# Optimization experiments

Hardware: AMD Instinct MI355X
Metric: run time of the kernel (lower is better)

Reference implementation:

```python
import jax, jax.numpy as jnp
import numpy as np
import math

SQ, SK, B, NP, HN = 2048, 2048, 2, 16, 128
LAYER_NUM = 1  # coeff
NORM_FACTOR = math.sqrt(2048 / 16) * LAYER_NUM  # sqrt(HIDDEN/HEADS) * coeff
SCALE = float(LAYER_NUM)  # MLSASoftmax scale


def setup_inputs() -> dict:
    key = jax.random.key(0)
    kq, kk, kv = jax.random.split(key, 3)
    query_layer = jax.random.normal(kq, (SQ, B, NP, HN), dtype=jnp.float32)
    key_layer = jax.random.normal(kk, (SK, B, NP, HN), dtype=jnp.float32)
    value_layer = jax.random.normal(kv, (SK, B, NP, HN), dtype=jnp.float32)
    # Causal mask: True = masked, shape [b, 1, sq, sk] (broadcasts over heads)
    causal = jnp.triu(jnp.ones((SQ, SK), dtype=bool), k=1)
    attention_mask = jnp.broadcast_to(causal[None, None], (B, 1, SQ, SK))
    return {
        "query_layer": query_layer,
        "key_layer": key_layer,
        "value_layer": value_layer,
        "attention_mask": attention_mask,
    }


def reference(query_layer, key_layer, value_layer, attention_mask):
    # scores[b,n,s,t] = (Q . K) / norm_factor, then * coeff in softmax
    scores = jnp.einsum("sbnh,tbnh->bnst", query_layer, key_layer) / NORM_FACTOR
    scores = scores * SCALE
    scores = jnp.where(attention_mask, jnp.float32(-10000.0), scores)
    # Module computes exp/sum WITHOUT max-subtraction; replicate exactly.
    exp_mo = jnp.exp(scores)
    denomi = jnp.sum(exp_mo, axis=-1, keepdims=True)  # [b, np, sq, 1]
    probs = exp_mo / denomi
    # dropout is identity in eval / for deterministic baseline
    ctx = jnp.einsum("bnst,tbnh->sbnh", probs, value_layer)  # [sq, b, np, hn]
    sq, b, n, h = ctx.shape
    context_layer = ctx.reshape(sq, b, n * h)
    return (context_layer, denomi)
```

## Files before the change

kernel.cpp:

```cpp
#include <hip/hip_runtime.h>
#include <hip/hip_bf16.h>
#include <stdint.h>

typedef __attribute__((ext_vector_type(8))) short short8;
typedef __attribute__((ext_vector_type(8))) unsigned short ushort8;
typedef __attribute__((ext_vector_type(4))) float f32x4;
typedef __attribute__((ext_vector_type(4))) int int4v;

#define NHEAD 32
#define SEQ   2048
#define HN    128

static constexpr float INV_NORM = 0.08838834764831845f;

__device__ __forceinline__ unsigned short f2bf(float f) {
  union { float f; unsigned u; } v; v.f = f;
  unsigned r = v.u + 0x7fffu + ((v.u >> 16) & 1u);
  return (unsigned short)(r >> 16);
}

__device__ __forceinline__ f32x4 mfma16(short8 a, short8 b, f32x4 c) {
  return __builtin_amdgcn_mfma_f32_16x16x32_bf16(a, b, c, 0, 0, 0);
}

__device__ __forceinline__ void gl_lds16(const void* g, void* l) {
  __builtin_amdgcn_global_load_lds(
      (const __attribute__((address_space(1))) unsigned int*)g,
      (__attribute__((address_space(3))) unsigned int*)l, 16, 0, 0);
}

__global__ __launch_bounds__(256) void prep_kv(const float* __restrict__ K,
                                               const float* __restrict__ V,
                                               unsigned short* __restrict__ kswz,
                                               unsigned short* __restrict__ vT) {
  __shared__ unsigned short lds[128 * 136];
  int bid = blockIdx.x;
  int tid = threadIdx.x;
  if (bid < 4096) {
    int idx = bid * 256 + tid;
    int cl = idx & 15;
    int t  = (idx >> 4) & 2047;
    int bn = idx >> 15;
    const float4* src = (const float4*)(K + ((size_t)t * 32 + bn) * 128 + cl * 8);
    float4 a = src[0], b = src[1];
    ushort8 o;
    o[0]=f2bf(a.x); o[1]=f2bf(a.y); o[2]=f2bf(a.z); o[3]=f2bf(a.w);
    o[4]=f2bf(b.x); o[5]=f2bf(b.y); o[6]=f2bf(b.z); o[7]=f2bf(b.w);
    *(ushort8*)(kswz + ((size_t)bn * 2048 + t) * 128 + ((cl ^ (t & 7)) * 8)) = o;
  } else {
    int vb = bid - 4096;
    int bn = vb >> 4;
    int t0 = (vb & 15) << 7;
    int r = tid >> 1, h0 = (tid & 1) * 64;
    const float* src = V + ((size_t)(t0 + r) * 32 + bn) * 128 + h0;
#pragma unroll
    for (int j = 0; j < 8; ++j) {
      float4 a = *(const float4*)(src + j * 8);
      float4 b = *(const float4*)(src + j * 8 + 4);
      ushort8 o;
      o[0]=f2bf(a.x); o[1]=f2bf(a.y); o[2]=f2bf(a.z); o[3]=f2bf(a.w);
      o[4]=f2bf(b.x); o[5]=f2bf(b.y); o[6]=f2bf(b.z); o[7]=f2bf(b.w);
      *(ushort8*)&lds[r * 136 + h0 + j * 8] = o;
    }
    __syncthreads();
    int h = tid >> 1, ts = (tid & 1) * 64;
    unsigned short tmp[64];
#pragma unroll
    for (int j = 0; j < 64; ++j) {
      int p = j & 31;
      int tloc = ((p >> 3) & 3) * 4 + ((p >> 2) & 1) * 16 + (p & 3);
      tmp[j] = lds[(ts + (j & 32) + tloc) * 136 + h];
    }
    ushort8* dst = (ushort8*)(vT + ((size_t)bn * 128 + h) * 2048 + t0 + ts);
#pragma unroll
    for (int j = 0; j < 8; ++j) dst[j] = *(ushort8*)&tmp[j * 8];
  }
}

template<bool BOTH>
__device__ __forceinline__ void half_tile(
    const char* kb, const char* vbh, int halfbase, int t0h, int qh, int ql,
    int l15, int hi, const short8 (&qf)[2][4],
    f32x4 (&acc)[2][8], float (&dacc)[2]) {
  f32x4 zz = {0.f, 0.f, 0.f, 0.f};
  int xr = (l15 & 7) << 4;
  short8 kf[2][4];
#pragma unroll
  for (int nt = 0; nt < 2; ++nt) {
    const char* krow = kb + (halfbase + nt * 16 + l15) * 256;
#pragma unroll
    for (int kk = 0; kk < 4; ++kk)
      kf[nt][kk] = *(const short8*)(krow + (((kk * 4 + hi) * 16) ^ xr));
  }
  f32x4 sH[2] = {zz, zz}, sL[2] = {zz, zz};
  __builtin_amdgcn_s_setprio(1);
#pragma unroll
  for (int nt = 0; nt < 2; ++nt)
#pragma unroll
    for (int kk = 0; kk < 4; ++kk) {
      sH[nt] = mfma16(kf[nt][kk], qf[0][kk], sH[nt]);
      if (BOTH) sL[nt] = mfma16(kf[nt][kk], qf[1][kk], sL[nt]);
    }
  __builtin_amdgcn_s_setprio(0);
  short8 vf[8];
#pragma unroll
  for (int ht = 0; ht < 8; ++ht)
    vf[ht] = *(const short8*)(vbh + (ht * 16 + l15) * 64 +
                              ((((l15 >> 1) + hi) & 3) * 16));
  auto pack = [&](float (&e)[8], float& da) -> short8 {
    da += ((e[0] + e[1]) + (e[2] + e[3])) + ((e[4] + e[5]) + (e[6] + e[7]));
    unsigned w0, w1, w2, w3;
    asm("v_cvt_pk_bf16_f32 %0, %1, %2" : "=v"(w0) : "v"(e[0]), "v"(e[1]));
    asm("v_cvt_pk_bf16_f32 %0, %1, %2" : "=v"(w1) : "v"(e[2]), "v"(e[3]));
    asm("v_cvt_pk_bf16_f32 %0, %1, %2" : "=v"(w2) : "v"(e[4]), "v"(e[5]));
    asm("v_cvt_pk_bf16_f32 %0, %1, %2" : "=v"(w3) : "v"(e[6]), "v"(e[7]));
    union { int4v u; short8 s; } pk;
    pk.u = (int4v){(int)w0, (int)w1, (int)w2, (int)w3};
    return pk.s;
  };
  auto softp_m = [&](f32x4* sv, int qbase, float& da) -> short8 {
    float e[8];
#pragma unroll
    for (int nt = 0; nt < 2; ++nt)
#pragma unroll
      for (int i = 0; i < 4; ++i) {
        float x = __expf(sv[nt][i] * INV_NORM);
        int kv = t0h + nt * 16 + hi * 4 + i;
        e[nt * 4 + i] = (kv <= qbase + l15) ? x : 0.0f;
      }
    return pack(e, da);
  };
  auto softp_u = [&](f32x4* sv, float& da) -> short8 {
    float e[8];
#pragma unroll
    for (int nt = 0; nt < 2; ++nt)
#pragma unroll
      for (int i = 0; i < 4; ++i)
        e[nt * 4 + i] = __expf(sv[nt][i] * INV_NORM);
    return pack(e, da);
  };
  bool maskH = (t0h + 31 > qh);
  short8 pH = maskH ? softp_m(sH, qh, dacc[0]) : softp_u(sH, dacc[0]);
  short8 pL = {};
  if (BOTH) {
    bool maskL = (t0h + 31 > ql);
    pL = maskL ? softp_m(sL, ql, dacc[1]) : softp_u(sL, dacc[1]);
  }
  __builtin_amdgcn_s_setprio(1);
#pragma unroll
  for (int ht = 0; ht < 8; ++ht) {
    acc[0][ht] = mfma16(pH, vf[ht], acc[0][ht]);
    if (BOTH) acc[1][ht] = mfma16(pL, vf[ht], acc[1][ht]);
  }
  __builtin_amdgcn_s_setprio(0);
}

__global__ __launch_bounds__(256, 2) void attn_main(const float* __restrict__ Q,
                                                    const unsigned short* __restrict__ kswz,
                                                    const unsigned short* __restrict__ vT,
                                                    float* __restrict__ out) {
  __shared__ char smem[65536];
  int tid = threadIdx.x;
  int lane = tid & 63;
  int w = tid >> 6;
  int l15 = lane & 15;
  int hi = lane >> 4;

  int bid = blockIdx.x;
  int bn = bid & 31;
  int x = bid >> 5;
  int p = (x < 8) ? x : 23 - x;
  int qtH = 31 - p, qtL = p;
  int qh = qtH * 64 + w * 16;
  int ql = qtL * 64 + w * 16;
  int ntile = qtH + 1;

  short8 qf[2][4];
#pragma unroll
  for (int qs = 0; qs < 2; ++qs) {
    int qbase = qs ? ql : qh;
    const float* qrow = Q + ((size_t)(qbase + l15) * 32 + bn) * 128;
#pragma unroll
    for (int kk = 0; kk < 4; ++kk) {
      float4 a = *(const float4*)(qrow + kk * 32 + hi * 8);
      float4 b = *(const float4*)(qrow + kk * 32 + hi * 8 + 4);
      short8 o;
      o[0]=(short)f2bf(a.x); o[1]=(short)f2bf(a.y);
      o[2]=(short)f2bf(a.z); o[3]=(short)f2bf(a.w);
      o[4]=(short)f2bf(b.x); o[5]=(short)f2bf(b.y);
      o[6]=(short)f2bf(b.z); o[7]=(short)f2bf(b.w);
      qf[qs][kk] = o;
    }
  }

  f32x4 zz = {0.f, 0.f, 0.f, 0.f};
  f32x4 acc[2][8];
#pragma unroll
  for (int qs = 0; qs < 2; ++qs)
#pragma unroll
    for (int ht = 0; ht < 8; ++ht) acc[qs][ht] = zz;
  float dacc[2] = {0.f, 0.f};

  const char* kg = (const char*)(kswz + (size_t)bn * 2048 * 128);
  const char* vg = (const char*)(vT + (size_t)bn * 128 * 2048);

  auto stage = [&](int buf, int t0) {
    const char* ksrc = kg + (size_t)t0 * 256;
    char* kl = smem + buf * 16384;
    int c = w * 64 + lane;
#pragma unroll
    for (int rr = 0; rr < 4; ++rr)
      gl_lds16(ksrc + (size_t)(c + rr * 256) * 16, kl + (c + rr * 256) * 16);
    char* vl = smem + 32768 + buf * 16384;
#pragma unroll
    for (int s = 0; s < 2; ++s)
#pragma unroll
      for (int rr = 0; rr < 2; ++rr) {
        int c2 = c + rr * 256;
        int h = c2 >> 2, sp = c2 & 3;
        int sl = (sp - (h >> 1)) & 3;
        gl_lds16(vg + (size_t)h * 4096 + (t0 + s * 32) * 2 + sl * 16,
                 vl + s * 8192 + c2 * 16);
      }
  };

  asm volatile("s_waitcnt vmcnt(0)" ::: "memory");
  stage(0, 0);

  int cur = 0;
  for (int it = 0; it < ntile; ++it) {
    int t0 = it * 64;
    asm volatile("s_waitcnt vmcnt(0)" ::: "memory");
    __builtin_amdgcn_s_barrier();
    if (it + 1 < ntile) stage(cur ^ 1, t0 + 64);

    const char* kb = smem + cur * 16384;
    const char* vb = smem + 32768 + cur * 16384;
#pragma unroll
    for (int half = 0; half < 2; ++half) {
      int t0h = t0 + half * 32;
      bool actL = (t0h <= ql + 15);
      bool actH = (t0h <= qh + 15);
      if (actL)
        half_tile<true>(kb, vb + half * 8192, half * 32, t0h, qh, ql,
                        l15, hi, qf, acc, dacc);
      else if (actH)
        half_tile<false>(kb, vb + half * 8192, half * 32, t0h, qh, ql,
                         l15, hi, qf, acc, dacc);
    }
    cur ^= 1;
  }

#pragma unroll
  for (int qs = 0; qs < 2; ++qs) {
    float d = dacc[qs];
    d += __shfl_xor(d, 16);
    d += __shfl_xor(d, 32);
    dacc[qs] = d;
  }
  float* dn = out + 8388608;
  if (hi == 0) {
    dn[(size_t)bn * 2048 + qh + l15] = dacc[0];
    dn[(size_t)bn * 2048 + ql + l15] = dacc[1];
  }
  float invH[4], invL[4];
#pragma unroll
  for (int i = 0; i < 4; ++i) {
    invH[i] = __builtin_amdgcn_rcpf(__shfl(dacc[0], hi * 4 + i));
    invL[i] = __builtin_amdgcn_rcpf(__shfl(dacc[1], hi * 4 + i));
  }

#pragma unroll
  for (int qs = 0; qs < 2; ++qs) {
    int qbase = qs ? ql : qh;
#pragma unroll
    for (int i = 0; i < 4; ++i) {
      float inv = qs ? invL[i] : invH[i];
      float* orow = out + (size_t)(qbase + hi * 4 + i) * 4096 + bn * 128 + l15;
#pragma unroll
      for (int ht = 0; ht < 8; ++ht)
        orow[ht * 16] = acc[qs][ht][i] * inv;
    }
  }
}

extern "C" void kernel_launch(void* const* d_in, const int* in_sizes, int n_in,
                              void* d_out, int out_size, void* d_ws, size_t ws_size,
                              hipStream_t stream) {
  const float* Q = (const float*)d_in[0];
  const float* K = (const float*)d_in[1];
  const float* V = (const float*)d_in[2];
  float* out = (float*)d_out;

  unsigned short* kswz = (unsigned short*)d_ws;
  unsigned short* vT   = kswz + (size_t)NHEAD * SEQ * HN;

  prep_kv<<<4608, 256, 0, stream>>>(K, V, kswz, vT);
  attn_main<<<512, 256, 0, stream>>>(Q, kswz, vT, out);
}
```

Before: 82.39 us.

## Split KV sequence across two wave groups per block and reduce partials in LDS

Doubles the block to 512 threads, with two groups of four waves each handling alternating 32-key half tiles of the same query rows, each with its own double-buffered LDS region. At the end the partial denominators and output accumulators are combined through shared memory before the normalized write. The aim is to raise the number of resident waves and hide latency within a block, in exchange for extra reduction traffic, more barriers, and heavier register pressure under the new launch bounds.

```diff
diff --git a/kernel.cpp b/kernel.cpp
--- a/kernel.cpp
+++ b/kernel.cpp
@@ -79,7 +79,7 @@
 
 template<bool BOTH>
 __device__ __forceinline__ void half_tile(
-    const char* kb, const char* vbh, int halfbase, int t0h, int qh, int ql,
+    const char* kb, const char* vbh, int t0h, int qh, int ql,
     int l15, int hi, const short8 (&qf)[2][4],
     f32x4 (&acc)[2][8], float (&dacc)[2]) {
   f32x4 zz = {0.f, 0.f, 0.f, 0.f};
@@ -87,7 +87,7 @@
   short8 kf[2][4];
 #pragma unroll
   for (int nt = 0; nt < 2; ++nt) {
-    const char* krow = kb + (halfbase + nt * 16 + l15) * 256;
+    const char* krow = kb + (nt * 16 + l15) * 256;
 #pragma unroll
     for (int kk = 0; kk < 4; ++kk)
       kf[nt][kk] = *(const short8*)(krow + (((kk * 4 + hi) * 16) ^ xr));
@@ -155,14 +155,16 @@
   __builtin_amdgcn_s_setprio(0);
 }
 
-__global__ __launch_bounds__(256, 2) void attn_main(const float* __restrict__ Q,
+__global__ __launch_bounds__(512, 4) void attn_main(const float* __restrict__ Q,
                                                     const unsigned short* __restrict__ kswz,
                                                     const unsigned short* __restrict__ vT,
                                                     float* __restrict__ out) {
   __shared__ char smem[65536];
   int tid = threadIdx.x;
   int lane = tid & 63;
-  int w = tid >> 6;
+  int w8 = tid >> 6;
+  int w = w8 & 3;
+  int sid = w8 >> 2;
   int l15 = lane & 15;
   int hi = lane >> 4;
 
@@ -173,7 +175,7 @@
   int qtH = 31 - p, qtL = p;
   int qh = qtH * 64 + w * 16;
   int ql = qtL * 64 + w * 16;
-  int ntile = qtH + 1;
+  int nIt = qtH + 1;
 
   short8 qf[2][4];
 #pragma unroll
@@ -204,52 +206,79 @@
   const char* kg = (const char*)(kswz + (size_t)bn * 2048 * 128);
   const char* vg = (const char*)(vT + (size_t)bn * 128 * 2048);
 
-  auto stage = [&](int buf, int t0) {
-    const char* ksrc = kg + (size_t)t0 * 256;
-    char* kl = smem + buf * 16384;
+  char* kbase = smem + sid * 16384;
+  char* vbase = smem + 32768 + sid * 16384;
+
+  auto stage = [&](int buf, int t) {
+    const char* ksrc = kg + (size_t)t * 8192;
+    char* kl = kbase + buf * 8192;
     int c = w * 64 + lane;
 #pragma unroll
-    for (int rr = 0; rr < 4; ++rr)
+    for (int rr = 0; rr < 2; ++rr)
       gl_lds16(ksrc + (size_t)(c + rr * 256) * 16, kl + (c + rr * 256) * 16);
-    char* vl = smem + 32768 + buf * 16384;
-#pragma unroll
-    for (int s = 0; s < 2; ++s)
-#pragma unroll
-      for (int rr = 0; rr < 2; ++rr) {
-        int c2 = c + rr * 256;
-        int h = c2 >> 2, sp = c2 & 3;
-        int sl = (sp - (h >> 1)) & 3;
-        gl_lds16(vg + (size_t)h * 4096 + (t0 + s * 32) * 2 + sl * 16,
-                 vl + s * 8192 + c2 * 16);
-      }
+    char* vl = vbase + buf * 8192;
+#pragma unroll
+    for (int rr = 0; rr < 2; ++rr) {
+      int c2 = c + rr * 256;
+      int h = c2 >> 2, sp = c2 & 3;
+      int sl = (sp - (h >> 1)) & 3;
+      gl_lds16(vg + (size_t)h * 4096 + (size_t)t * 64 + sl * 16,
+               vl + c2 * 16);
+    }
   };
 
   asm volatile("s_waitcnt vmcnt(0)" ::: "memory");
-  stage(0, 0);
+  stage(0, sid);
 
   int cur = 0;
-  for (int it = 0; it < ntile; ++it) {
-    int t0 = it * 64;
+  for (int it = 0; it < nIt; ++it) {
+    int t = it * 2 + sid;
     asm volatile("s_waitcnt vmcnt(0)" ::: "memory");
     __builtin_amdgcn_s_barrier();
-    if (it + 1 < ntile) stage(cur ^ 1, t0 + 64);
-
-    const char* kb = smem + cur * 16384;
-    const char* vb = smem + 32768 + cur * 16384;
-#pragma unroll
-    for (int half = 0; half < 2; ++half) {
-      int t0h = t0 + half * 32;
-      bool actL = (t0h <= ql + 15);
-      bool actH = (t0h <= qh + 15);
-      if (actL)
-        half_tile<true>(kb, vb + half * 8192, half * 32, t0h, qh, ql,
-                        l15, hi, qf, acc, dacc);
-      else if (actH)
-        half_tile<false>(kb, vb + half * 8192, half * 32, t0h, qh, ql,
-                         l15, hi, qf, acc, dacc);
-    }
+    if (it + 1 < nIt) stage(cur ^ 1, t + 2);
+
+    int t0h = t * 32;
+    const char* kb = kbase + cur * 8192;
+    const char* vbh = vbase + cur * 8192;
+    bool actL = (t0h <= ql + 15);
+    bool actH = (t0h <= qh + 15);
+    if (actL)
+      half_tile<true>(kb, vbh, t0h, qh, ql, l15, hi, qf, acc, dacc);
+    else if (actH)
+      half_tile<false>(kb, vbh, t0h, qh, ql, l15, hi, qf, acc, dacc);
     cur ^= 1;
   }
+
+  __syncthreads();
+  float* dsm = (float*)smem;
+  if (sid == 1) {
+    dsm[0 * 256 + w * 64 + lane] = dacc[0];
+    dsm[1 * 256 + w * 64 + lane] = dacc[1];
+  }
+  __syncthreads();
+  if (sid == 0) {
+    dacc[0] += dsm[0 * 256 + w * 64 + lane];
+    dacc[1] += dsm[1 * 256 + w * 64 + lane];
+  }
+  __syncthreads();
+  f32x4* accsm = (f32x4*)smem;
+  if (sid == 1) {
+#pragma unroll
+    for (int qs = 0; qs < 2; ++qs)
+#pragma unroll
+      for (int ht = 0; ht < 8; ++ht)
+        accsm[(qs * 8 + ht) * 256 + w * 64 + lane] = acc[qs][ht];
+  }
+  __syncthreads();
+  if (sid == 1) return;
+#pragma unroll
+  for (int qs = 0; qs < 2; ++qs)
+#pragma unroll
+    for (int ht = 0; ht < 8; ++ht) {
+      f32x4 o = accsm[(qs * 8 + ht) * 256 + w * 64 + lane];
+      acc[qs][ht][0] += o[0]; acc[qs][ht][1] += o[1];
+      acc[qs][ht][2] += o[2]; acc[qs][ht][3] += o[3];
+    }
 
 #pragma unroll
   for (int qs = 0; qs < 2; ++qs) {
@@ -296,5 +325,5 @@
   unsigned short* vT   = kswz + (size_t)NHEAD * SEQ * HN;
 
   prep_kv<<<4608, 256, 0, stream>>>(K, V, kswz, vT);
-  attn_main<<<512, 256, 0, stream>>>(Q, kswz, vT, out);
-}
+  attn_main<<<512, 512, 0, stream>>>(Q, kswz, vT, out);
+}
```

New measurement: 255.0 us. 3.1x slower.

## Interleave QK and PV MFMAs across two half-tiles and fold scale into Q

Applied to the files above, without the earlier changes.

Adds a tile64 path that processes both 32-key halves of a 64-key tile together, computing the second half's QK scores while the first half's softmax and PV MFMAs run. This lets exp/pack work overlap with matrix ops. The first K fragment is now read from LDS before the next async stage is issued. The 1/sqrt(d) scale is folded into Q before its bf16 conversion, which removes a multiply per score but changes rounding slightly. Register pressure rises from holding two score sets and two V fragment sets, which may hurt occupancy at launch bounds of 2.

```diff
diff --git a/kernel.cpp b/kernel.cpp
--- a/kernel.cpp
+++ b/kernel.cpp
@@ -77,21 +77,70 @@
   }
 }
 
+__device__ __forceinline__ void read_kf(const char* kb, int base, int l15, int hi,
+                                        short8 (&kf)[2][4]) {
+  int xr = (l15 & 7) << 4;
+#pragma unroll
+  for (int nt = 0; nt < 2; ++nt) {
+    const char* krow = kb + (base + nt * 16 + l15) * 256;
+#pragma unroll
+    for (int kk = 0; kk < 4; ++kk)
+      kf[nt][kk] = *(const short8*)(krow + (((kk * 4 + hi) * 16) ^ xr));
+  }
+}
+
+__device__ __forceinline__ void read_vf(const char* vbh, int l15, int hi,
+                                        short8 (&vf)[8]) {
+#pragma unroll
+  for (int ht = 0; ht < 8; ++ht)
+    vf[ht] = *(const short8*)(vbh + (ht * 16 + l15) * 64 +
+                              ((((l15 >> 1) + hi) & 3) * 16));
+}
+
+__device__ __forceinline__ short8 packp(const float (&e)[8], float& da) {
+  da += ((e[0] + e[1]) + (e[2] + e[3])) + ((e[4] + e[5]) + (e[6] + e[7]));
+  unsigned w0, w1, w2, w3;
+  asm("v_cvt_pk_bf16_f32 %0, %1, %2" : "=v"(w0) : "v"(e[0]), "v"(e[1]));
+  asm("v_cvt_pk_bf16_f32 %0, %1, %2" : "=v"(w1) : "v"(e[2]), "v"(e[3]));
+  asm("v_cvt_pk_bf16_f32 %0, %1, %2" : "=v"(w2) : "v"(e[4]), "v"(e[5]));
+  asm("v_cvt_pk_bf16_f32 %0, %1, %2" : "=v"(w3) : "v"(e[6]), "v"(e[7]));
+  union { int4v u; short8 s; } pk;
+  pk.u = (int4v){(int)w0, (int)w1, (int)w2, (int)w3};
+  return pk.s;
+}
+
+__device__ __forceinline__ short8 softp_m(const f32x4 (&sv)[2], int t0h, int qbase,
+                                          int l15, int hi, float& da) {
+  float e[8];
+#pragma unroll
+  for (int nt = 0; nt < 2; ++nt)
+#pragma unroll
+    for (int i = 0; i < 4; ++i) {
+      float x = __expf(sv[nt][i]);
+      int kv = t0h + nt * 16 + hi * 4 + i;
+      e[nt * 4 + i] = (kv <= qbase + l15) ? x : 0.0f;
+    }
+  return packp(e, da);
+}
+
+__device__ __forceinline__ short8 softp_u(const f32x4 (&sv)[2], float& da) {
+  float e[8];
+#pragma unroll
+  for (int nt = 0; nt < 2; ++nt)
+#pragma unroll
+    for (int i = 0; i < 4; ++i)
+      e[nt * 4 + i] = __expf(sv[nt][i]);
+  return packp(e, da);
+}
+
 template<bool BOTH>
 __device__ __forceinline__ void half_tile(
     const char* kb, const char* vbh, int halfbase, int t0h, int qh, int ql,
     int l15, int hi, const short8 (&qf)[2][4],
     f32x4 (&acc)[2][8], float (&dacc)[2]) {
   f32x4 zz = {0.f, 0.f, 0.f, 0.f};
-  int xr = (l15 & 7) << 4;
   short8 kf[2][4];
-#pragma unroll
-  for (int nt = 0; nt < 2; ++nt) {
-    const char* krow = kb + (halfbase + nt * 16 + l15) * 256;
-#pragma unroll
-    for (int kk = 0; kk < 4; ++kk)
-      kf[nt][kk] = *(const short8*)(krow + (((kk * 4 + hi) * 16) ^ xr));
-  }
+  read_kf(kb, halfbase, l15, hi, kf);
   f32x4 sH[2] = {zz, zz}, sL[2] = {zz, zz};
   __builtin_amdgcn_s_setprio(1);
 #pragma unroll
@@ -103,54 +152,82 @@
     }
   __builtin_amdgcn_s_setprio(0);
   short8 vf[8];
-#pragma unroll
-  for (int ht = 0; ht < 8; ++ht)
-    vf[ht] = *(const short8*)(vbh + (ht * 16 + l15) * 64 +
-                              ((((l15 >> 1) + hi) & 3) * 16));
-  auto pack = [&](float (&e)[8], float& da) -> short8 {
-    da += ((e[0] + e[1]) + (e[2] + e[3])) + ((e[4] + e[5]) + (e[6] + e[7]));
-    unsigned w0, w1, w2, w3;
-    asm("v_cvt_pk_bf16_f32 %0, %1, %2" : "=v"(w0) : "v"(e[0]), "v"(e[1]));
-    asm("v_cvt_pk_bf16_f32 %0, %1, %2" : "=v"(w1) : "v"(e[2]), "v"(e[3]));
-    asm("v_cvt_pk_bf16_f32 %0, %1, %2" : "=v"(w2) : "v"(e[4]), "v"(e[5]));
-    asm("v_cvt_pk_bf16_f32 %0, %1, %2" : "=v"(w3) : "v"(e[6]), "v"(e[7]));
-    union { int4v u; short8 s; } pk;
-    pk.u = (int4v){(int)w0, (int)w1, (int)w2, (int)w3};
-    return pk.s;
-  };
-  auto softp_m = [&](f32x4* sv, int qbase, float& da) -> short8 {
-    float e[8];
-#pragma unroll
-    for (int nt = 0; nt < 2; ++nt)
-#pragma unroll
-      for (int i = 0; i < 4; ++i) {
-        float x = __expf(sv[nt][i] * INV_NORM);
-        int kv = t0h + nt * 16 + hi * 4 + i;
-        e[nt * 4 + i] = (kv <= qbase + l15) ? x : 0.0f;
-      }
-    return pack(e, da);
-  };
-  auto softp_u = [&](f32x4* sv, float& da) -> short8 {
-    float e[8];
-#pragma unroll
-    for (int nt = 0; nt < 2; ++nt)
-#pragma unroll
-      for (int i = 0; i < 4; ++i)
-        e[nt * 4 + i] = __expf(sv[nt][i] * INV_NORM);
-    return pack(e, da);
-  };
+  read_vf(vbh, l15, hi, vf);
   bool maskH = (t0h + 31 > qh);
-  short8 pH = maskH ? softp_m(sH, qh, dacc[0]) : softp_u(sH, dacc[0]);
+  short8 pH = maskH ? softp_m(sH, t0h, qh, l15, hi, dacc[0]) : softp_u(sH, dacc[0]);
   short8 pL = {};
   if (BOTH) {
     bool maskL = (t0h + 31 > ql);
-    pL = maskL ? softp_m(sL, ql, dacc[1]) : softp_u(sL, dacc[1]);
+    pL = maskL ? softp_m(sL, t0h, ql, l15, hi, dacc[1]) : softp_u(sL, dacc[1]);
   }
   __builtin_amdgcn_s_setprio(1);
 #pragma unroll
   for (int ht = 0; ht < 8; ++ht) {
     acc[0][ht] = mfma16(pH, vf[ht], acc[0][ht]);
     if (BOTH) acc[1][ht] = mfma16(pL, vf[ht], acc[1][ht]);
+  }
+  __builtin_amdgcn_s_setprio(0);
+}
+
+template<bool BOTH>
+__device__ __forceinline__ void tile64(
+    const char* kb, const char* vb, int t0, int qh, int ql,
+    int l15, int hi, const short8 (&qf)[2][4], const short8 (&kf0)[2][4],
+    f32x4 (&acc)[2][8], float (&dacc)[2]) {
+  f32x4 zz = {0.f, 0.f, 0.f, 0.f};
+  f32x4 sH0[2] = {zz, zz}, sL0[2] = {zz, zz};
+  __builtin_amdgcn_s_setprio(1);
+#pragma unroll
+  for (int nt = 0; nt < 2; ++nt)
+#pragma unroll
+    for (int kk = 0; kk < 4; ++kk) {
+      sH0[nt] = mfma16(kf0[nt][kk], qf[0][kk], sH0[nt]);
+      if (BOTH) sL0[nt] = mfma16(kf0[nt][kk], qf[1][kk], sL0[nt]);
+    }
+  __builtin_amdgcn_s_setprio(0);
+  short8 kf1[2][4];
+  read_kf(kb, 32, l15, hi, kf1);
+  short8 vf0[8];
+  read_vf(vb, l15, hi, vf0);
+  f32x4 sH1[2] = {zz, zz}, sL1[2] = {zz, zz};
+  __builtin_amdgcn_s_setprio(1);
+#pragma unroll
+  for (int nt = 0; nt < 2; ++nt)
+#pragma unroll
+    for (int kk = 0; kk < 4; ++kk) {
+      sH1[nt] = mfma16(kf1[nt][kk], qf[0][kk], sH1[nt]);
+      if (BOTH) sL1[nt] = mfma16(kf1[nt][kk], qf[1][kk], sL1[nt]);
+    }
+  bool mH0 = (t0 + 31 > qh);
+  short8 pH0 = mH0 ? softp_m(sH0, t0, qh, l15, hi, dacc[0]) : softp_u(sH0, dacc[0]);
+  short8 pL0 = {};
+  if (BOTH) {
+    bool mL0 = (t0 + 31 > ql);
+    pL0 = mL0 ? softp_m(sL0, t0, ql, l15, hi, dacc[1]) : softp_u(sL0, dacc[1]);
+  }
+  __builtin_amdgcn_s_setprio(0);
+  short8 vf1[8];
+  read_vf(vb + 8192, l15, hi, vf1);
+  int t1 = t0 + 32;
+  __builtin_amdgcn_s_setprio(1);
+#pragma unroll
+  for (int ht = 0; ht < 8; ++ht) {
+    acc[0][ht] = mfma16(pH0, vf0[ht], acc[0][ht]);
+    if (BOTH) acc[1][ht] = mfma16(pL0, vf0[ht], acc[1][ht]);
+  }
+  bool mH1 = (t1 + 31 > qh);
+  short8 pH1 = mH1 ? softp_m(sH1, t1, qh, l15, hi, dacc[0]) : softp_u(sH1, dacc[0]);
+  short8 pL1 = {};
+  if (BOTH) {
+    bool mL1 = (t1 + 31 > ql);
+    pL1 = mL1 ? softp_m(sL1, t1, ql, l15, hi, dacc[1]) : softp_u(sL1, dacc[1]);
+  }
+  __builtin_amdgcn_s_setprio(0);
+  __builtin_amdgcn_s_setprio(1);
+#pragma unroll
+  for (int ht = 0; ht < 8; ++ht) {
+    acc[0][ht] = mfma16(pH1, vf1[ht], acc[0][ht]);
+    if (BOTH) acc[1][ht] = mfma16(pL1, vf1[ht], acc[1][ht]);
   }
   __builtin_amdgcn_s_setprio(0);
 }
@@ -185,10 +262,10 @@
       float4 a = *(const float4*)(qrow + kk * 32 + hi * 8);
       float4 b = *(const float4*)(qrow + kk * 32 + hi * 8 + 4);
       short8 o;
-      o[0]=(short)f2bf(a.x); o[1]=(short)f2bf(a.y);
-      o[2]=(short)f2bf(a.z); o[3]=(short)f2bf(a.w);
-      o[4]=(short)f2bf(b.x); o[5]=(short)f2bf(b.y);
-      o[6]=(short)f2bf(b.z); o[7]=(short)f2bf(b.w);
+      o[0]=(short)f2bf(a.x*INV_NORM); o[1]=(short)f2bf(a.y*INV_NORM);
+      o[2]=(short)f2bf(a.z*INV_NORM); o[3]=(short)f2bf(a.w*INV_NORM);
+      o[4]=(short)f2bf(b.x*INV_NORM); o[5]=(short)f2bf(b.y*INV_NORM);
+      o[6]=(short)f2bf(b.z*INV_NORM); o[7]=(short)f2bf(b.w*INV_NORM);
       qf[qs][kk] = o;
     }
   }
@@ -232,21 +309,33 @@
     int t0 = it * 64;
     asm volatile("s_waitcnt vmcnt(0)" ::: "memory");
     __builtin_amdgcn_s_barrier();
-    if (it + 1 < ntile) stage(cur ^ 1, t0 + 64);
 
     const char* kb = smem + cur * 16384;
     const char* vb = smem + 32768 + cur * 16384;
-#pragma unroll
-    for (int half = 0; half < 2; ++half) {
-      int t0h = t0 + half * 32;
-      bool actL = (t0h <= ql + 15);
-      bool actH = (t0h <= qh + 15);
-      if (actL)
-        half_tile<true>(kb, vb + half * 8192, half * 32, t0h, qh, ql,
-                        l15, hi, qf, acc, dacc);
-      else if (actH)
-        half_tile<false>(kb, vb + half * 8192, half * 32, t0h, qh, ql,
-                         l15, hi, qf, acc, dacc);
+    bool L0 = (t0 <= ql + 15);
+    bool L1 = (t0 + 32 <= ql + 15);
+    bool H1 = (t0 + 32 <= qh + 15);
+
+    if (L1 || (!L0 && H1)) {
+      short8 kf0[2][4];
+      read_kf(kb, 0, l15, hi, kf0);
+      if (it + 1 < ntile) stage(cur ^ 1, t0 + 64);
+      if (L1) tile64<true>(kb, vb, t0, qh, ql, l15, hi, qf, kf0, acc, dacc);
+      else    tile64<false>(kb, vb, t0, qh, ql, l15, hi, qf, kf0, acc, dacc);
+    } else {
+      if (it + 1 < ntile) stage(cur ^ 1, t0 + 64);
+#pragma unroll
+      for (int half = 0; half < 2; ++half) {
+        int t0h = t0 + half * 32;
+        bool actL = (t0h <= ql + 15);
+        bool actH = (t0h <= qh + 15);
+        if (actL)
+          half_tile<true>(kb, vb + half * 8192, half * 32, t0h, qh, ql,
+                          l15, hi, qf, acc, dacc);
+        else if (actH)
+          half_tile<false>(kb, vb + half * 8192, half * 32, t0h, qh, ql,
+                           l15, hi, qf, acc, dacc);
+      }
     }
     cur ^= 1;
   }
```

Result: no change. 82.70 us (+0.4%).

## Split paired query tiles into single-tile blocks with smaller LDS and higher occupancy

Applied to the files above, without the earlier changes.

Each block previously handled a causal-balanced pair of query tiles (high and low) using 64-row K/V stages. Now each block handles one 64-row query tile with 32-key stages. Grid size doubles, LDS is halved, and launch bounds allow 4 blocks per CU. The block order is arranged so the longest tiles launch first, replacing the old pairing for load balance. The softmax scale is folded into Q at load, and the K fragment read is moved ahead of issuing the next stage. The cost is that each K/V tile is now loaded twice as often per query row and there are more barriers per unit of work.

```diff
diff --git a/kernel.cpp b/kernel.cpp
--- a/kernel.cpp
+++ b/kernel.cpp
@@ -77,89 +77,67 @@
   }
 }
 
-template<bool BOTH>
-__device__ __forceinline__ void half_tile(
-    const char* kb, const char* vbh, int halfbase, int t0h, int qh, int ql,
-    int l15, int hi, const short8 (&qf)[2][4],
-    f32x4 (&acc)[2][8], float (&dacc)[2]) {
-  f32x4 zz = {0.f, 0.f, 0.f, 0.f};
+__device__ __forceinline__ void read_kf(const char* kb, int l15, int hi,
+                                        short8 (&kf)[2][4]) {
   int xr = (l15 & 7) << 4;
-  short8 kf[2][4];
 #pragma unroll
   for (int nt = 0; nt < 2; ++nt) {
-    const char* krow = kb + (halfbase + nt * 16 + l15) * 256;
+    const char* krow = kb + (nt * 16 + l15) * 256;
 #pragma unroll
     for (int kk = 0; kk < 4; ++kk)
       kf[nt][kk] = *(const short8*)(krow + (((kk * 4 + hi) * 16) ^ xr));
   }
-  f32x4 sH[2] = {zz, zz}, sL[2] = {zz, zz};
-  __builtin_amdgcn_s_setprio(1);
-#pragma unroll
-  for (int nt = 0; nt < 2; ++nt)
-#pragma unroll
-    for (int kk = 0; kk < 4; ++kk) {
-      sH[nt] = mfma16(kf[nt][kk], qf[0][kk], sH[nt]);
-      if (BOTH) sL[nt] = mfma16(kf[nt][kk], qf[1][kk], sL[nt]);
-    }
-  __builtin_amdgcn_s_setprio(0);
-  short8 vf[8];
+}
+
+__device__ __forceinline__ void read_vf(const char* vbh, int l15, int hi,
+                                        short8 (&vf)[8]) {
 #pragma unroll
   for (int ht = 0; ht < 8; ++ht)
     vf[ht] = *(const short8*)(vbh + (ht * 16 + l15) * 64 +
                               ((((l15 >> 1) + hi) & 3) * 16));
-  auto pack = [&](float (&e)[8], float& da) -> short8 {
-    da += ((e[0] + e[1]) + (e[2] + e[3])) + ((e[4] + e[5]) + (e[6] + e[7]));
-    unsigned w0, w1, w2, w3;
-    asm("v_cvt_pk_bf16_f32 %0, %1, %2" : "=v"(w0) : "v"(e[0]), "v"(e[1]));
-    asm("v_cvt_pk_bf16_f32 %0, %1, %2" : "=v"(w1) : "v"(e[2]), "v"(e[3]));
-    asm("v_cvt_pk_bf16_f32 %0, %1, %2" : "=v"(w2) : "v"(e[4]), "v"(e[5]));
-    asm("v_cvt_pk_bf16_f32 %0, %1, %2" : "=v"(w3) : "v"(e[6]), "v"(e[7]));
-    union { int4v u; short8 s; } pk;
-    pk.u = (int4v){(int)w0, (int)w1, (int)w2, (int)w3};
-    return pk.s;
-  };
-  auto softp_m = [&](f32x4* sv, int qbase, float& da) -> short8 {
-    float e[8];
-#pragma unroll
-    for (int nt = 0; nt < 2; ++nt)
-#pragma unroll
-      for (int i = 0; i < 4; ++i) {
-        float x = __expf(sv[nt][i] * INV_NORM);
-        int kv = t0h + nt * 16 + hi * 4 + i;
-        e[nt * 4 + i] = (kv <= qbase + l15) ? x : 0.0f;
-      }
-    return pack(e, da);
-  };
-  auto softp_u = [&](f32x4* sv, float& da) -> short8 {
-    float e[8];
-#pragma unroll
-    for (int nt = 0; nt < 2; ++nt)
-#pragma unroll
-      for (int i = 0; i < 4; ++i)
-        e[nt * 4 + i] = __expf(sv[nt][i] * INV_NORM);
-    return pack(e, da);
-  };
-  bool maskH = (t0h + 31 > qh);
-  short8 pH = maskH ? softp_m(sH, qh, dacc[0]) : softp_u(sH, dacc[0]);
-  short8 pL = {};
-  if (BOTH) {
-    bool maskL = (t0h + 31 > ql);
-    pL = maskL ? softp_m(sL, ql, dacc[1]) : softp_u(sL, dacc[1]);
-  }
-  __builtin_amdgcn_s_setprio(1);
-#pragma unroll
-  for (int ht = 0; ht < 8; ++ht) {
-    acc[0][ht] = mfma16(pH, vf[ht], acc[0][ht]);
-    if (BOTH) acc[1][ht] = mfma16(pL, vf[ht], acc[1][ht]);
-  }
-  __builtin_amdgcn_s_setprio(0);
-}
-
-__global__ __launch_bounds__(256, 2) void attn_main(const float* __restrict__ Q,
+}
+
+__device__ __forceinline__ short8 packp(const float (&e)[8], float& da) {
+  da += ((e[0] + e[1]) + (e[2] + e[3])) + ((e[4] + e[5]) + (e[6] + e[7]));
+  unsigned w0, w1, w2, w3;
+  asm("v_cvt_pk_bf16_f32 %0, %1, %2" : "=v"(w0) : "v"(e[0]), "v"(e[1]));
+  asm("v_cvt_pk_bf16_f32 %0, %1, %2" : "=v"(w1) : "v"(e[2]), "v"(e[3]));
+  asm("v_cvt_pk_bf16_f32 %0, %1, %2" : "=v"(w2) : "v"(e[4]), "v"(e[5]));
+  asm("v_cvt_pk_bf16_f32 %0, %1, %2" : "=v"(w3) : "v"(e[6]), "v"(e[7]));
+  union { int4v u; short8 s; } pk;
+  pk.u = (int4v){(int)w0, (int)w1, (int)w2, (int)w3};
+  return pk.s;
+}
+
+__device__ __forceinline__ short8 softp_m(const f32x4 (&sv)[2], int t0h, int qbase,
+                                          int l15, int hi, float& da) {
+  float e[8];
+#pragma unroll
+  for (int nt = 0; nt < 2; ++nt)
+#pragma unroll
+    for (int i = 0; i < 4; ++i) {
+      float x = __expf(sv[nt][i]);
+      int kv = t0h + nt * 16 + hi * 4 + i;
+      e[nt * 4 + i] = (kv <= qbase + l15) ? x : 0.0f;
+    }
+  return packp(e, da);
+}
+
+__device__ __forceinline__ short8 softp_u(const f32x4 (&sv)[2], float& da) {
+  float e[8];
+#pragma unroll
+  for (int nt = 0; nt < 2; ++nt)
+#pragma unroll
+    for (int i = 0; i < 4; ++i)
+      e[nt * 4 + i] = __expf(sv[nt][i]);
+  return packp(e, da);
+}
+
+__global__ __launch_bounds__(256, 4) void attn_main(const float* __restrict__ Q,
                                                     const unsigned short* __restrict__ kswz,
                                                     const unsigned short* __restrict__ vT,
                                                     float* __restrict__ out) {
-  __shared__ char smem[65536];
+  __shared__ char smem[32768];
   int tid = threadIdx.x;
   int lane = tid & 63;
   int w = tid >> 6;
@@ -168,60 +146,53 @@
 
   int bid = blockIdx.x;
   int bn = bid & 31;
-  int x = bid >> 5;
-  int p = (x < 8) ? x : 23 - x;
-  int qtH = 31 - p, qtL = p;
-  int qh = qtH * 64 + w * 16;
-  int ql = qtL * 64 + w * 16;
-  int ntile = qtH + 1;
-
-  short8 qf[2][4];
-#pragma unroll
-  for (int qs = 0; qs < 2; ++qs) {
-    int qbase = qs ? ql : qh;
-    const float* qrow = Q + ((size_t)(qbase + l15) * 32 + bn) * 128;
+  int z = bid >> 5;
+  int g = z & 7, s = z >> 3;
+  int qt = (s == 0) ? (31 - g) : (s == 1) ? (16 + g) : (s == 2) ? (15 - g) : g;
+  int qb = qt * 64 + w * 16;
+  int ntile = 2 * qt + 2;
+
+  short8 qf[4];
+  {
+    const float* qrow = Q + ((size_t)(qb + l15) * 32 + bn) * 128;
 #pragma unroll
     for (int kk = 0; kk < 4; ++kk) {
       float4 a = *(const float4*)(qrow + kk * 32 + hi * 8);
       float4 b = *(const float4*)(qrow + kk * 32 + hi * 8 + 4);
       short8 o;
-      o[0]=(short)f2bf(a.x); o[1]=(short)f2bf(a.y);
-      o[2]=(short)f2bf(a.z); o[3]=(short)f2bf(a.w);
-      o[4]=(short)f2bf(b.x); o[5]=(short)f2bf(b.y);
-      o[6]=(short)f2bf(b.z); o[7]=(short)f2bf(b.w);
-      qf[qs][kk] = o;
+      o[0]=(short)f2bf(a.x*INV_NORM); o[1]=(short)f2bf(a.y*INV_NORM);
+      o[2]=(short)f2bf(a.z*INV_NORM); o[3]=(short)f2bf(a.w*INV_NORM);
+      o[4]=(short)f2bf(b.x*INV_NORM); o[5]=(short)f2bf(b.y*INV_NORM);
+      o[6]=(short)f2bf(b.z*INV_NORM); o[7]=(short)f2bf(b.w*INV_NORM);
+      qf[kk] = o;
     }
   }
 
   f32x4 zz = {0.f, 0.f, 0.f, 0.f};
-  f32x4 acc[2][8];
-#pragma unroll
-  for (int qs = 0; qs < 2; ++qs)
-#pragma unroll
-    for (int ht = 0; ht < 8; ++ht) acc[qs][ht] = zz;
-  float dacc[2] = {0.f, 0.f};
+  f32x4 acc[8];
+#pragma unroll
+  for (int ht = 0; ht < 8; ++ht) acc[ht] = zz;
+  float dacc = 0.f;
 
   const char* kg = (const char*)(kswz + (size_t)bn * 2048 * 128);
   const char* vg = (const char*)(vT + (size_t)bn * 128 * 2048);
 
-  auto stage = [&](int buf, int t0) {
-    const char* ksrc = kg + (size_t)t0 * 256;
-    char* kl = smem + buf * 16384;
+  auto stage = [&](int buf, int t) {
+    const char* ksrc = kg + (size_t)t * 8192;
+    char* kl = smem + buf * 8192;
     int c = w * 64 + lane;
 #pragma unroll
-    for (int rr = 0; rr < 4; ++rr)
+    for (int rr = 0; rr < 2; ++rr)
       gl_lds16(ksrc + (size_t)(c + rr * 256) * 16, kl + (c + rr * 256) * 16);
-    char* vl = smem + 32768 + buf * 16384;
-#pragma unroll
-    for (int s = 0; s < 2; ++s)
-#pragma unroll
-      for (int rr = 0; rr < 2; ++rr) {
-        int c2 = c + rr * 256;
-        int h = c2 >> 2, sp = c2 & 3;
-        int sl = (sp - (h >> 1)) & 3;
-        gl_lds16(vg + (size_t)h * 4096 + (t0 + s * 32) * 2 + sl * 16,
-                 vl + s * 8192 + c2 * 16);
-      }
+    char* vl = smem + 16384 + buf * 8192;
+#pragma unroll
+    for (int rr = 0; rr < 2; ++rr) {
+      int c2 = c + rr * 256;
+      int h = c2 >> 2, sp = c2 & 3;
+      int sl = (sp - (h >> 1)) & 3;
+      gl_lds16(vg + (size_t)h * 4096 + (size_t)t * 64 + sl * 16,
+               vl + c2 * 16);
+    }
   };
 
   asm volatile("s_waitcnt vmcnt(0)" ::: "memory");
@@ -229,58 +200,61 @@
 
   int cur = 0;
   for (int it = 0; it < ntile; ++it) {
-    int t0 = it * 64;
+    int t0h = it * 32;
     asm volatile("s_waitcnt vmcnt(0)" ::: "memory");
     __builtin_amdgcn_s_barrier();
-    if (it + 1 < ntile) stage(cur ^ 1, t0 + 64);
-
-    const char* kb = smem + cur * 16384;
-    const char* vb = smem + 32768 + cur * 16384;
-#pragma unroll
-    for (int half = 0; half < 2; ++half) {
-      int t0h = t0 + half * 32;
-      bool actL = (t0h <= ql + 15);
-      bool actH = (t0h <= qh + 15);
-      if (actL)
-        half_tile<true>(kb, vb + half * 8192, half * 32, t0h, qh, ql,
-                        l15, hi, qf, acc, dacc);
-      else if (actH)
-        half_tile<false>(kb, vb + half * 8192, half * 32, t0h, qh, ql,
-                         l15, hi, qf, acc, dacc);
+
+    const char* kb = smem + cur * 8192;
+    const char* vbh = smem + 16384 + cur * 8192;
+    bool act = (t0h <= qb + 15);
+
+    short8 kf[2][4];
+    if (act) read_kf(kb, l15, hi, kf);
+    if (it + 1 < ntile) stage(cur ^ 1, it + 1);
+
+    if (act) {
+      f32x4 sv[2] = {zz, zz};
+      __builtin_amdgcn_s_setprio(1);
+#pragma unroll
+      for (int nt = 0; nt < 2; ++nt)
+#pragma unroll
+        for (int kk = 0; kk < 4; ++kk)
+          sv[nt] = mfma16(kf[nt][kk], qf[kk], sv[nt]);
+      __builtin_amdgcn_s_setprio(0);
+      short8 vf[8];
+      read_vf(vbh, l15, hi, vf);
+      bool mask = (t0h + 31 > qb);
+      short8 p = mask ? softp_m(sv, t0h, qb, l15, hi, dacc)
+                      : softp_u(sv, dacc);
+      __builtin_amdgcn_s_setprio(1);
+#pragma unroll
+      for (int ht = 0; ht < 8; ++ht)
+        acc[ht] = mfma16(p, vf[ht], acc[ht]);
+      __builtin_amdgcn_s_setprio(0);
     }
     cur ^= 1;
   }
 
-#pragma unroll
-  for (int qs = 0; qs < 2; ++qs) {
-    float d = dacc[qs];
+  {
+    float d = dacc;
     d += __shfl_xor(d, 16);
     d += __shfl_xor(d, 32);
-    dacc[qs] = d;
+    dacc = d;
   }
   float* dn = out + 8388608;
-  if (hi == 0) {
-    dn[(size_t)bn * 2048 + qh + l15] = dacc[0];
-    dn[(size_t)bn * 2048 + ql + l15] = dacc[1];
-  }
-  float invH[4], invL[4];
+  if (hi == 0) dn[(size_t)bn * 2048 + qb + l15] = dacc;
+
+  float inv[4];
+#pragma unroll
+  for (int i = 0; i < 4; ++i)
+    inv[i] = __builtin_amdgcn_rcpf(__shfl(dacc, hi * 4 + i));
+
 #pragma unroll
   for (int i = 0; i < 4; ++i) {
-    invH[i] = __builtin_amdgcn_rcpf(__shfl(dacc[0], hi * 4 + i));
-    invL[i] = __builtin_amdgcn_rcpf(__shfl(dacc[1], hi * 4 + i));
-  }
-
-#pragma unroll
-  for (int qs = 0; qs < 2; ++qs) {
-    int qbase = qs ? ql : qh;
-#pragma unroll
-    for (int i = 0; i < 4; ++i) {
-      float inv = qs ? invL[i] : invH[i];
-      float* orow = out + (size_t)(qbase + hi * 4 + i) * 4096 + bn * 128 + l15;
-#pragma unroll
-      for (int ht = 0; ht < 8; ++ht)
-        orow[ht * 16] = acc[qs][ht][i] * inv;
-    }
+    float* orow = out + (size_t)(qb + hi * 4 + i) * 4096 + bn * 128 + l15;
+#pragma unroll
+    for (int ht = 0; ht < 8; ++ht)
+      orow[ht * 16] = acc[ht][i] * inv[i];
   }
 }
 
@@ -296,5 +270,5 @@
   unsigned short* vT   = kswz + (size_t)NHEAD * SEQ * HN;
 
   prep_kv<<<4608, 256, 0, stream>>>(K, V, kswz, vT);
-  attn_main<<<512, 256, 0, stream>>>(Q, kswz, vT, out);
-}
+  attn_main<<<1024, 256, 0, stream>>>(Q, kswz, vT, out);
+}
```

After: 181.5 us. +120.3%, slower.
